# Kernel tuning notes

Measured on AMD Instinct MI355X. Metric: run time of the kernel, lower is better.

The kernel has to match this reference:

```python
import jax, jax.numpy as jnp
import numpy as np

EPS = 1e-6  # flax nn.LayerNorm default epsilon


def excl_cumsum(a, axis):
    c = jnp.roll(jnp.cumsum(a, axis=axis), 1, axis=axis)
    idx = [slice(None)] * a.ndim
    idx[axis] = slice(0, 1)
    return c.at[tuple(idx)].set(0.0)


def mixed_chunk_attn(q, k, v, n_chunks):
    # Mixed chunk linear attention (https://arxiv.org/pdf/2202.10447.pdf)
    if n_chunks == 1:
        mask = jnp.tri(q.shape[1], q.shape[1], -1, dtype=q.dtype)
        qk = jnp.einsum('bls,bms->blm', q, k) * mask
        return jnp.einsum('blm,bme->ble', qk, v)
    B, L = q.shape[:2]
    C = L // n_chunks
    qc = q.reshape(B, n_chunks, C, -1)
    kc = k.reshape(B, n_chunks, C, -1)
    vc = v.reshape(B, n_chunks, C, -1)
    # global linear attention across chunks (exclusive prefix of kv states)
    kv = excl_cumsum(jnp.einsum('bgcs,bgce->bgse', kc, vc), axis=1)
    glob = jnp.einsum('bgcs,bgse->bgce', qc, kv)
    # local strictly-causal quadratic attention within each chunk
    mask = jnp.tri(C, C, -1, dtype=q.dtype)
    qk = jnp.einsum('bgns,bgms->bgnm', qc, kc) * mask
    loc = jnp.einsum('bgnm,bgme->bgne', qk, vc)
    return (glob + loc).reshape(B, L, -1)


def ln_normalize(x):
    mu = jnp.mean(x, axis=-1, keepdims=True)
    var = jnp.mean(jnp.square(x - mu), axis=-1, keepdims=True)
    return (x - mu) * jax.lax.rsqrt(var + EPS)


def fwblock(x, labels, weights, W1, b1, W2, b2, ln_scale, ln_bias, Wu, bu, step_sizes, n_chunks):
    B, L, D = x.shape
    F = W1.shape[1]

    # slow-weight forward with zero perturbations; grad wrt perturbations gives
    # per-token gradients at each layer's output (rank-one fast-weight updates).
    def slow_loss(p1, p3, p_scale, p_bias):
        h1 = x @ W1 + b1 + p1                    # FWDense(4D) + output perturbation
        h2 = jnp.square(jax.nn.relu(h1))         # FWSquaredRelu (paramless)
        h3 = h2 @ W2 + b2 + p3                   # FWDense(D) + output perturbation
        h4 = ln_normalize(h3) * (ln_scale + p_scale) + (ln_bias + p_bias)
        logits = h4 @ Wu + bu
        ll = -jnp.sum(jax.nn.log_softmax(logits) * labels, axis=-1)
        loss = jnp.sum(weights * ll) / jnp.maximum(jnp.sum(weights), 1e-8)
        return loss, h2

    zeros = (jnp.zeros((B, L, F), x.dtype), jnp.zeros((B, L, D), x.dtype),
             jnp.zeros((B, L, D), x.dtype), jnp.zeros((B, L, D), x.dtype))
    (g1, g3, g_scale, g_bias), h2_slow = jax.grad(
        slow_loss, argnums=(0, 1, 2, 3), has_aux=True)(*zeros)

    # fast-weight forward: rank-one weight updates expressed as causal linear attn
    x1 = x @ W1 + b1 - step_sizes[0] * mixed_chunk_attn(x, x, g1, n_chunks)
    x2 = jnp.square(jax.nn.relu(x1))             # step_sizes[1] unused (no params)
    x3 = x2 @ W2 + b2 - step_sizes[2] * mixed_chunk_attn(x2, h2_slow, g3, n_chunks)
    fast_scale = ln_scale - step_sizes[3] * excl_cumsum(g_scale, axis=1)
    fast_bias = ln_bias - step_sizes[3] * excl_cumsum(g_bias, axis=1)
    x4 = ln_normalize(x3) * fast_scale + fast_bias
    return x4 @ Wu + bu


def setup_inputs():
    key = jax.random.key(0)
    ks = jax.random.split(key, 6)
    B, L, D, V = 2, 2048, 1024, 8192
    F = 4 * D
    x = jax.random.normal(ks[0], (B, L, D), jnp.float32)
    labels = jax.random.uniform(ks[1], (B, L, V), jnp.float32)
    weights = jnp.ones((B, L), jnp.float32)
    W1 = jax.random.normal(ks[2], (D, F), jnp.float32) / np.sqrt(D).astype(np.float32)
    b1 = jnp.zeros((F,), jnp.float32)
    W2 = jax.random.normal(ks[3], (F, D), jnp.float32) / np.sqrt(F).astype(np.float32)
    b2 = jnp.zeros((D,), jnp.float32)
    ln_scale = jnp.ones((D,), jnp.float32)
    ln_bias = jnp.zeros((D,), jnp.float32)
    Wu = jax.random.normal(ks[4], (D, V), jnp.float32) / np.sqrt(D).astype(np.float32)
    bu = jnp.zeros((V,), jnp.float32)
    step_sizes = jnp.full((4,), 0.01, jnp.float32)
    return dict(x=x, labels=labels, weights=weights, W1=W1, b1=b1, W2=W2, b2=b2,
                ln_scale=ln_scale, ln_bias=ln_bias, Wu=Wu, bu=bu,
                step_sizes=step_sizes, n_chunks=16)


def reference(x, labels, weights, W1, b1, W2, b2, ln_scale, ln_bias, Wu, bu, step_sizes, n_chunks):
    return fwblock(x, labels, weights, W1, b1, W2, b2, ln_scale, ln_bias, Wu, bu, step_sizes, n_chunks)
```

## Files before the change

kernel.cpp:

```cpp
#include <hip/hip_runtime.h>
#include <cstdint>

typedef unsigned short ushort_t;
typedef __bf16 bf16x8 __attribute__((ext_vector_type(8)));
typedef float f32x4 __attribute__((ext_vector_type(4)));

__device__ __forceinline__ ushort_t f2bf(float f) {
  union { float f; unsigned int u; } v; v.f = f;
  unsigned int u = v.u;
  unsigned int r = (u + 0x7fffu + ((u >> 16) & 1u)) >> 16;
  return (ushort_t)r;
}
__device__ __forceinline__ float bf2f(ushort_t u) {
  union { unsigned int u; float f; } v; v.u = ((unsigned int)u) << 16; return v.f;
}

#define GLOAD16(gp, lp)                                                              \
  __builtin_amdgcn_global_load_lds(                                                  \
      reinterpret_cast<const __attribute__((address_space(1))) unsigned int*>(       \
          reinterpret_cast<uintptr_t>(gp)),                                          \
      reinterpret_cast<__attribute__((address_space(3))) unsigned int*>(             \
          reinterpret_cast<uintptr_t>(lp)),                                          \
      16, 0, 0)

struct GemmP {
  const ushort_t* A; const ushort_t* B;
  int M, N, K;
  long long sA, sB;
  float* outf;   long long sOutF;
  ushort_t* outb; long long sOutB;
  ushort_t* outb2;
  const float* bias;
  const float* auxf; long long sAuxF;
  const ushort_t* auxb;
  const float* steps;
  float* part; int ksplit, Kc, Tt;
};

template <int EPI>
__global__ __launch_bounds__(256) void gemm_bt(GemmP p) {
  const int nwg = gridDim.x * gridDim.y;
  const int orig = blockIdx.y * gridDim.x + blockIdx.x;
  const int xcd = orig & 7, loc = orig >> 3;
  const int q = nwg >> 3, r = nwg & 7;
  const int wg = (xcd < r) ? (xcd * (q + 1) + loc) : (r * (q + 1) + (xcd - r) * q + loc);
  int mt, nt;
  if (EPI == 7) {
    int t_ = wg;
    mt = (int)((sqrtf(8.f * t_ + 1.f) - 1.f) * 0.5f);
    while ((mt + 1) * (mt + 2) / 2 <= t_) mt++;
    while (mt * (mt + 1) / 2 > t_) mt--;
    nt = t_ - mt * (mt + 1) / 2;
  } else {
    nt = wg % gridDim.x; mt = wg / gridDim.x;
  }
  const int m0 = mt * 128, n0 = nt * 128;

  int bz = blockIdx.z, ks = 0;
  if (EPI == 6 || EPI == 7) { bz = blockIdx.z / p.ksplit; ks = blockIdx.z % p.ksplit; }

  const ushort_t* A = p.A + (size_t)bz * p.sA;
  const ushort_t* B = p.B + (size_t)bz * p.sB;

  int kbeg = 0, kend = p.K;
  if (EPI == 6 || EPI == 7) { kbeg = ks * p.Kc; kend = kbeg + p.Kc; }
  else if (EPI == 4 || EPI == 5) kend = min(p.K, m0 + 128);

  __shared__ ushort_t sA[3 * 128 * 32];
  __shared__ ushort_t sB[3 * 128 * 32];

  const int tid = threadIdx.x;
  const int wid = tid >> 6, lane = tid & 63;
  const int wm = wid >> 1, wn = wid & 1;

  f32x4 acc[4][4];
#pragma unroll
  for (int i = 0; i < 4; i++)
#pragma unroll
    for (int j = 0; j < 4; j++) acc[i][j] = f32x4{0.f, 0.f, 0.f, 0.f};

  const int lr = lane >> 2;
  const int lc = (lane & 3) * 8;
  const int rA0 = wid * 16 + lr;
  const int rA1 = 64 + wid * 16 + lr;
  const ushort_t* gA0 = A + (size_t)(m0 + rA0) * p.K + lc;
  const ushort_t* gA1 = A + (size_t)(m0 + rA1) * p.K + lc;
  const ushort_t* gB0 = B + (size_t)(n0 + rA0) * p.K + lc;
  const ushort_t* gB1 = B + (size_t)(n0 + rA1) * p.K + lc;
  ushort_t* lA0 = &sA[wid * 512];
  ushort_t* lA1 = &sA[(4 + wid) * 512];
  ushort_t* lB0 = &sB[wid * 512];
  ushort_t* lB1 = &sB[(4 + wid) * 512];

  const int fr = lane & 15;
  const int kb = (lane >> 4) * 8;

  const int nIter = (kend - kbeg) >> 5;
  auto stage = [&](int t, int buf) {
    const int kk = kbeg + t * 32;
    const int o = buf * 4096;
    GLOAD16(gA0 + kk, lA0 + o);
    GLOAD16(gA1 + kk, lA1 + o);
    GLOAD16(gB0 + kk, lB0 + o);
    GLOAD16(gB1 + kk, lB1 + o);
  };
  stage(0, 0);
  if (nIter > 1) stage(1, 1);

  for (int t = 0; t < nIter; ++t) {
    if (t + 1 < nIter) { asm volatile("s_waitcnt vmcnt(4)" ::: "memory"); }
    else               { asm volatile("s_waitcnt vmcnt(0)" ::: "memory"); }
    __builtin_amdgcn_s_barrier();
    __builtin_amdgcn_sched_barrier(0);
    if (t + 2 < nIter) stage(t + 2, (t + 2) % 3);
    const int co = (t % 3) * 4096;
    bf16x8 av[4], bv[4];
#pragma unroll
    for (int i = 0; i < 4; i++) {
      av[i] = *reinterpret_cast<const bf16x8*>(&sA[co + (wm * 64 + i * 16 + fr) * 32 + kb]);
      bv[i] = *reinterpret_cast<const bf16x8*>(&sB[co + (wn * 64 + i * 16 + fr) * 32 + kb]);
    }
#pragma unroll
    for (int i = 0; i < 4; i++)
#pragma unroll
      for (int j = 0; j < 4; j++)
        acc[i][j] = __builtin_amdgcn_mfma_f32_16x16x32_bf16(av[i], bv[j], acc[i][j], 0, 0, 0);
  }

  const int fq = lane >> 4;
  float ss = 0.f;
  if (EPI == 4) ss = p.steps[0];
  else if (EPI == 5) ss = p.steps[2];
  float* outf = p.outf ? p.outf + (size_t)bz * p.sOutF : nullptr;
  ushort_t* outb = p.outb ? p.outb + (size_t)bz * p.sOutB : nullptr;
  ushort_t* outb2 = p.outb2;
  const float* auxf = p.auxf ? p.auxf + (size_t)bz * p.sAuxF : nullptr;
  const ushort_t* auxb = p.auxb ? p.auxb + (size_t)bz * p.sAuxF : nullptr;
  float* partT = nullptr;
  if (EPI == 6) partT = p.part + (size_t)blockIdx.z * p.M * p.N;
  if (EPI == 7) partT = p.part + ((size_t)blockIdx.z * p.Tt + wg) * 16384;

#pragma unroll
  for (int i = 0; i < 4; i++) {
#pragma unroll
    for (int j = 0; j < 4; j++) {
#pragma unroll
      for (int r2 = 0; r2 < 4; r2++) {
        int lrow = wm * 64 + i * 16 + fq * 4 + r2;
        int lcol = wn * 64 + j * 16 + fr;
        int row = m0 + lrow, col = n0 + lcol;
        size_t g = (size_t)row * p.N + col;
        float v = acc[i][j][r2];
        if (EPI == 0) {
          outf[g] = v + (p.bias ? p.bias[col] : 0.f);
        } else if (EPI == 8) {
          outb[g] = f2bf(v + p.bias[col]);
        } else if (EPI == 1) {
          v += p.bias[col];
          outb[g] = f2bf(v);
          float rl = fmaxf(v, 0.f);
          outb2[g] = f2bf(rl * rl);
        } else if (EPI == 2) {
          outb[g] = f2bf(v * 2.f * sqrtf(bf2f(p.auxb[g])));
        } else if (EPI == 4) {
          float x1 = bf2f(auxb[g]) - ss * v;
          float rl = fmaxf(x1, 0.f);
          outb[g] = f2bf(rl * rl);
        } else if (EPI == 5) {
          outf[g] = auxf[g] - ss * v;
        } else if (EPI == 6) {
          partT[g] = v;
        } else if (EPI == 7) {
          partT[lrow * 128 + lcol] = v;
        }
      }
    }
  }
}

__global__ __launch_bounds__(256) void k_comb(const float* part, const float* bias, float* out,
                                              int N, size_t MN, int S) {
  size_t e = ((size_t)blockIdx.x * 256 + threadIdx.x) * 4;
  if (e >= MN) return;
  float4 s = *(const float4*)(part + e);
  for (int p_ = 1; p_ < S; p_++) {
    float4 v = *(const float4*)(part + (size_t)p_ * MN + e);
    s.x += v.x; s.y += v.y; s.z += v.z; s.w += v.w;
  }
  if (bias) {
    int col = (int)(e % (size_t)N);
    s.x += bias[col]; s.y += bias[col + 1]; s.z += bias[col + 2]; s.w += bias[col + 3];
  }
  *(float4*)(out + e) = s;
}

__global__ __launch_bounds__(256) void k_combtri(const float* part, ushort_t* out, int Tt, int S,
                                                 int L) {
  int t = blockIdx.x, bz = blockIdx.y;
  int mt = (int)((sqrtf(8.f * t + 1.f) - 1.f) * 0.5f);
  while ((mt + 1) * (mt + 2) / 2 <= t) mt++;
  while (mt * (mt + 1) / 2 > t) mt--;
  int nt = t - mt * (mt + 1) / 2;
  const float* pb = part + ((size_t)bz * S * Tt + t) * 16384;
  ushort_t* ob = out + (size_t)bz * L * L;
  for (int e4 = threadIdx.x; e4 < 4096; e4 += 256) {
    int e = e4 * 4;
    float4 s = *(const float4*)(pb + e);
    for (int p_ = 1; p_ < S; p_++) {
      float4 v = *(const float4*)(pb + (size_t)p_ * Tt * 16384 + e);
      s.x += v.x; s.y += v.y; s.z += v.z; s.w += v.w;
    }
    int lr = e >> 7, lc2 = e & 127;
    int row = mt * 128 + lr, col = nt * 128 + lc2;
    ushort4 o;
    o.x = (col < row) ? f2bf(s.x) : (ushort_t)0;
    o.y = (col + 1 < row) ? f2bf(s.y) : (ushort_t)0;
    o.z = (col + 2 < row) ? f2bf(s.z) : (ushort_t)0;
    o.w = (col + 3 < row) ? f2bf(s.w) : (ushort_t)0;
    *(ushort4*)(&ob[(size_t)row * L + col]) = o;
  }
}

__global__ __launch_bounds__(256) void k_conv(const float* in, ushort_t* out, size_t n) {
  size_t i = ((size_t)blockIdx.x * 256 + threadIdx.x) * 4;
  if (i >= n) return;
  float4 v = *(const float4*)(in + i);
  out[i] = f2bf(v.x); out[i + 1] = f2bf(v.y); out[i + 2] = f2bf(v.z); out[i + 3] = f2bf(v.w);
}

__global__ __launch_bounds__(256) void k_tconv(const float* in, ushort_t* out, int R, int C) {
  __shared__ float t[32][33];
  int c0 = blockIdx.x * 32, r0 = blockIdx.y * 32;
  int tx = threadIdx.x & 31, ty = threadIdx.x >> 5;
#pragma unroll
  for (int i = ty; i < 32; i += 8) t[i][tx] = in[(size_t)(r0 + i) * C + c0 + tx];
  __syncthreads();
#pragma unroll
  for (int i = ty; i < 32; i += 8) out[(size_t)(c0 + i) * R + r0 + tx] = f2bf(t[tx][i]);
}

__global__ __launch_bounds__(256) void k_tb2b(const ushort_t* in, ushort_t* out, int L, int C) {
  __shared__ ushort_t t[32][33];
  int b = blockIdx.z;
  const ushort_t* ib = in + (size_t)b * L * C;
  ushort_t* ob = out + (size_t)b * C * L;
  int c0 = blockIdx.x * 32, l0 = blockIdx.y * 32;
  int tx = threadIdx.x & 31, ty = threadIdx.x >> 5;
#pragma unroll
  for (int i = ty; i < 32; i += 8) t[i][tx] = ib[(size_t)(l0 + i) * C + c0 + tx];
  __syncthreads();
#pragma unroll
  for (int i = ty; i < 32; i += 8) ob[(size_t)(c0 + i) * L + l0 + tx] = t[tx][i];
}

__device__ __forceinline__ void blockRed2(float& a, float& b, float* red) {
#pragma unroll
  for (int o = 32; o; o >>= 1) { a += __shfl_down(a, o); b += __shfl_down(b, o); }
  int w = threadIdx.x >> 6;
  if ((threadIdx.x & 63) == 0) { red[w] = a; red[4 + w] = b; }
  __syncthreads();
  a = red[0] + red[1] + red[2] + red[3];
  b = red[4] + red[5] + red[6] + red[7];
  __syncthreads();
}

__global__ __launch_bounds__(256) void k_lnfwd(const float* X, const float* sc, const float* bi,
                                               float* nout, float* rstd, ushort_t* yb, int D) {
  __shared__ float red[8];
  int row = blockIdx.x;
  const float* x = X + (size_t)row * D;
  float s = 0.f, s2 = 0.f;
  for (int d = threadIdx.x; d < D; d += 256) { float v = x[d]; s += v; s2 += v * v; }
  blockRed2(s, s2, red);
  float mu = s / D;
  float var = s2 / D - mu * mu;
  float rs = rsqrtf(var + 1e-6f);
  for (int d = threadIdx.x; d < D; d += 256) {
    float nv = (x[d] - mu) * rs;
    nout[(size_t)row * D + d] = nv;
    yb[(size_t)row * D + d] = f2bf(nv * sc[d] + bi[d]);
  }
  if (threadIdx.x == 0) rstd[row] = rs;
}

__global__ __launch_bounds__(256) void k_lnfwd2(const float* X, const float* fs, const float* fb,
                                                ushort_t* yb, int D) {
  __shared__ float red[8];
  int row = blockIdx.x;
  const float* x = X + (size_t)row * D;
  float s = 0.f, s2 = 0.f;
  for (int d = threadIdx.x; d < D; d += 256) { float v = x[d]; s += v; s2 += v * v; }
  blockRed2(s, s2, red);
  float mu = s / D;
  float var = s2 / D - mu * mu;
  float rs = rsqrtf(var + 1e-6f);
  for (int d = threadIdx.x; d < D; d += 256) {
    size_t g = (size_t)row * D + d;
    float nv = (x[d] - mu) * rs;
    yb[g] = f2bf(nv * fs[g] + fb[g]);
  }
}

__global__ __launch_bounds__(256) void k_lnbwd(const float* G, const float* nn, const float* rstd,
                                               const float* sc, ushort_t* g3b, float* gsc, int D) {
  __shared__ float red[8];
  int row = blockIdx.x;
  const float* g = G + (size_t)row * D;
  const float* n_ = nn + (size_t)row * D;
  float sa = 0.f, sb = 0.f;
  for (int d = threadIdx.x; d < D; d += 256) {
    float dn = g[d] * sc[d];
    sa += dn; sb += dn * n_[d];
  }
  blockRed2(sa, sb, red);
  float a = sa / D, b = sb / D, rs = rstd[row];
  for (int d = threadIdx.x; d < D; d += 256) {
    size_t gi = (size_t)row * D + d;
    float dn = g[d] * sc[d];
    g3b[gi] = f2bf(rs * (dn - a - n_[d] * b));
    gsc[gi] = g[d] * n_[d];
  }
}

__global__ __launch_bounds__(256) void k_wsum(const float* w, float* o, int n) {
  __shared__ float red[4];
  float s = 0.f;
  for (int i = threadIdx.x; i < n; i += 256) s += w[i];
#pragma unroll
  for (int d = 32; d; d >>= 1) s += __shfl_down(s, d);
  if ((threadIdx.x & 63) == 0) red[threadIdx.x >> 6] = s;
  __syncthreads();
  if (threadIdx.x == 0) o[0] = fmaxf(red[0] + red[1] + red[2] + red[3], 1e-8f);
}

__global__ __launch_bounds__(256) void k_softgrad(const ushort_t* logits, const float* labels,
                                                  const float* w, const float* wsum,
                                                  ushort_t* dlb, int V) {
  __shared__ float lrow[8192];
  __shared__ float red[8];
  int row = blockIdx.x;
  const ushort_t* l = logits + (size_t)row * V;
  const float* y = labels + (size_t)row * V;
  float m = -3.4e38f, t = 0.f;
  for (int v = threadIdx.x; v < V; v += 256) {
    float lv = bf2f(l[v]);
    lrow[v] = lv;
    m = fmaxf(m, lv);
    t += y[v];
  }
#pragma unroll
  for (int o = 32; o; o >>= 1) { m = fmaxf(m, __shfl_down(m, o)); t += __shfl_down(t, o); }
  int wv = threadIdx.x >> 6;
  if ((threadIdx.x & 63) == 0) { red[wv] = m; red[4 + wv] = t; }
  __syncthreads();
  m = fmaxf(fmaxf(red[0], red[1]), fmaxf(red[2], red[3]));
  t = red[4] + red[5] + red[6] + red[7];
  __syncthreads();
  float s = 0.f;
  for (int v = threadIdx.x; v < V; v += 256) s += expf(lrow[v] - m);
#pragma unroll
  for (int o = 32; o; o >>= 1) s += __shfl_down(s, o);
  if ((threadIdx.x & 63) == 0) red[wv] = s;
  __syncthreads();
  s = red[0] + red[1] + red[2] + red[3];
  float c = w[row] / wsum[0];
  float invs = 1.f / s;
  for (int v = threadIdx.x; v < V; v += 256) {
    size_t g = (size_t)row * V + v;
    dlb[g] = f2bf(c * (expf(lrow[v] - m) * invs * t - y[v]));
  }
}

__global__ __launch_bounds__(256) void k_scanpart(const float* gs, const float* gb, float* ps,
                                                  float* pb, int L, int D) {
  int d = blockIdx.x * 256 + threadIdx.x;
  int seg = blockIdx.y, b = blockIdx.z;
  const int SEGL = L / 16;
  size_t base = ((size_t)b * L + seg * SEGL) * D + d;
  float s1 = 0.f, s2 = 0.f;
  for (int i = 0; i < SEGL; i++) { s1 += gs[base + (size_t)i * D]; s2 += gb[base + (size_t)i * D]; }
  size_t pi = ((size_t)b * 16 + seg) * D + d;
  ps[pi] = s1; pb[pi] = s2;
}

__global__ __launch_bounds__(256) void k_scanapply(const float* gs, const float* gb,
                                                   const float* ps, const float* pb,
                                                   const float* sc, const float* bi,
                                                   const float* steps, float* fs, float* fb,
                                                   int L, int D) {
  int d = blockIdx.x * 256 + threadIdx.x;
  int seg = blockIdx.y, b = blockIdx.z;
  const int SEGL = L / 16;
  float ss = steps[3];
  float rs_ = 0.f, rb_ = 0.f;
  for (int s = 0; s < seg; s++) {
    size_t pi = ((size_t)b * 16 + s) * D + d;
    rs_ += ps[pi]; rb_ += pb[pi];
  }
  float s0 = sc[d], b0 = bi[d];
  size_t base = ((size_t)b * L + seg * SEGL) * D + d;
  for (int i = 0; i < SEGL; i++) {
    size_t g = base + (size_t)i * D;
    fs[g] = s0 - ss * rs_;
    fb[g] = b0 - ss * rb_;
    rs_ += gs[g]; rb_ += gb[g];
  }
}

extern "C" void kernel_launch(void* const* d_in, const int* in_sizes, int n_in, void* d_out,
                              int out_size, void* d_ws, size_t ws_size, hipStream_t stream) {
  const float* x        = (const float*)d_in[0];
  const float* labels   = (const float*)d_in[1];
  const float* weights  = (const float*)d_in[2];
  const float* W1       = (const float*)d_in[3];
  const float* b1       = (const float*)d_in[4];
  const float* W2       = (const float*)d_in[5];
  const float* b2       = (const float*)d_in[6];
  const float* ln_scale = (const float*)d_in[7];
  const float* ln_bias  = (const float*)d_in[8];
  const float* Wu       = (const float*)d_in[9];
  const float* bu       = (const float*)d_in[10];
  const float* steps    = (const float*)d_in[11];

  const int BL = in_sizes[2];
  const int D  = in_sizes[7];
  const int F  = in_sizes[4];
  const int V  = in_sizes[10];
  const int Bb = 2, L = BL / Bb;
  const int Tt = (L / 128) * (L / 128 + 1) / 2;

  char* ws = (char*)d_ws;
  size_t off = 0;
  auto take = [&](size_t b) { char* p = ws + off; off = (off + b + 255) & ~(size_t)255; return p; };

  ushort_t* xb   = (ushort_t*)take((size_t)BL * D * 2);
  ushort_t* w1t  = (ushort_t*)take((size_t)F * D * 2);
  ushort_t* w2t  = (ushort_t*)take((size_t)D * F * 2);
  ushort_t* w2b  = (ushort_t*)take((size_t)F * D * 2);
  ushort_t* wut  = (ushort_t*)take((size_t)V * D * 2);
  ushort_t* wub  = (ushort_t*)take((size_t)D * V * 2);
  ushort_t* H1b  = (ushort_t*)take((size_t)BL * F * 2);
  ushort_t* H2b  = (ushort_t*)take((size_t)BL * F * 2);
  float*    H3   = (float*)take((size_t)BL * D * 4);
  float*    nbuf = (float*)take((size_t)BL * D * 4);
  float*    rstd = (float*)take((size_t)BL * 4);
  ushort_t* h4b  = (ushort_t*)take((size_t)BL * D * 2);
  float*    wsumb= (float*)take(256);
  float*    G4   = (float*)take((size_t)BL * D * 4);
  float*    gsc  = (float*)take((size_t)BL * D * 4);
  ushort_t* g3b  = (ushort_t*)take((size_t)BL * D * 2);
  ushort_t* g3t  = (ushort_t*)take((size_t)BL * D * 2);
  float*    fs   = (float*)take((size_t)BL * D * 4);
  float*    fb   = (float*)take((size_t)BL * D * 4);
  ushort_t* x4b  = (ushort_t*)take((size_t)BL * D * 2);
  float*    psc  = (float*)take((size_t)Bb * 16 * D * 4);
  float*    pbi  = (float*)take((size_t)Bb * 16 * D * 4);
  char* poolA = take((size_t)BL * V * 4);
  ushort_t* logitsb = (ushort_t*)poolA;
  float*    partA  = (float*)poolA;
  ushort_t* g1b = (ushort_t*)poolA;
  ushort_t* g1t = (ushort_t*)(poolA + (size_t)BL * F * 2);
  ushort_t* S1b = (ushort_t*)(poolA + (size_t)BL * F * 4);
  ushort_t* x2b = (ushort_t*)(poolA + (size_t)BL * F * 4 + (size_t)Bb * L * L * 2);
  char* poolB = take((size_t)BL * V * 2);
  ushort_t* dlb = (ushort_t*)poolB;
  float*    partS1 = (float*)poolB;
  ushort_t* S2b = (ushort_t*)poolB;
  float*    X3  = (float*)(poolB + (size_t)Bb * L * L * 2);
  float*    x3  = (float*)(poolB + (size_t)Bb * L * L * 2 + (size_t)BL * D * 4);

  dim3 blk(256);
  const size_t MN_D = (size_t)BL * D;

  k_conv<<<dim3((unsigned)((size_t)BL * D / 1024)), blk, 0, stream>>>(x, xb, (size_t)BL * D);
  k_tconv<<<dim3(F / 32, D / 32), blk, 0, stream>>>(W1, w1t, D, F);
  k_tconv<<<dim3(D / 32, F / 32), blk, 0, stream>>>(W2, w2t, F, D);
  k_conv<<<dim3((unsigned)((size_t)F * D / 1024)), blk, 0, stream>>>(W2, w2b, (size_t)F * D);
  k_tconv<<<dim3(V / 32, D / 32), blk, 0, stream>>>(Wu, wut, D, V);
  k_conv<<<dim3((unsigned)((size_t)D * V / 1024)), blk, 0, stream>>>(Wu, wub, (size_t)D * V);

  GemmP p;
  auto clr = [&]() { p = GemmP{}; };

  clr(); p.A = xb; p.B = w1t; p.M = BL; p.N = F; p.K = D;
  p.outb = H1b; p.outb2 = H2b; p.bias = b1;
  gemm_bt<1><<<dim3(F / 128, BL / 128, 1), blk, 0, stream>>>(p);
  clr(); p.A = H2b; p.B = w2t; p.M = BL; p.N = D; p.K = F;
  p.part = partA; p.ksplit = 4; p.Kc = F / 4;
  gemm_bt<6><<<dim3(D / 128, BL / 128, 4), blk, 0, stream>>>(p);
  k_comb<<<dim3((unsigned)(MN_D / 1024)), blk, 0, stream>>>(partA, b2, H3, D, MN_D, 4);
  k_lnfwd<<<dim3(BL), blk, 0, stream>>>(H3, ln_scale, ln_bias, nbuf, rstd, h4b, D);
  clr(); p.A = h4b; p.B = wut; p.M = BL; p.N = V; p.K = D; p.outb = logitsb; p.bias = bu;
  gemm_bt<8><<<dim3(V / 128, BL / 128, 1), blk, 0, stream>>>(p);
  k_wsum<<<dim3(1), blk, 0, stream>>>(weights, wsumb, BL);
  k_softgrad<<<dim3(BL), blk, 0, stream>>>(logitsb, labels, weights, wsumb, dlb, V);
  clr(); p.A = dlb; p.B = wub; p.M = BL; p.N = D; p.K = V;
  p.part = partA; p.ksplit = 4; p.Kc = V / 4;
  gemm_bt<6><<<dim3(D / 128, BL / 128, 4), blk, 0, stream>>>(p);
  k_comb<<<dim3((unsigned)(MN_D / 1024)), blk, 0, stream>>>(partA, nullptr, G4, D, MN_D, 4);
  k_lnbwd<<<dim3(BL), blk, 0, stream>>>(G4, nbuf, rstd, ln_scale, g3b, gsc, D);
  clr(); p.A = g3b; p.B = w2b; p.M = BL; p.N = F; p.K = D; p.outb = g1b; p.auxb = H2b;
  gemm_bt<2><<<dim3(F / 128, BL / 128, 1), blk, 0, stream>>>(p);
  k_tb2b<<<dim3(F / 32, L / 32, Bb), blk, 0, stream>>>(g1b, g1t, L, F);
  k_tb2b<<<dim3(D / 32, L / 32, Bb), blk, 0, stream>>>(g3b, g3t, L, D);
  clr(); p.A = xb; p.B = xb; p.M = L; p.N = L; p.K = D;
  p.sA = (long long)L * D; p.sB = (long long)L * D;
  p.part = partS1; p.ksplit = 2; p.Kc = D / 2; p.Tt = Tt;
  gemm_bt<7><<<dim3(Tt, 1, Bb * 2), blk, 0, stream>>>(p);
  k_combtri<<<dim3(Tt, Bb), blk, 0, stream>>>(partS1, S1b, Tt, 2, L);
  clr(); p.A = S1b; p.B = g1t; p.M = L; p.N = F; p.K = L;
  p.sA = (long long)L * L; p.sB = (long long)F * L;
  p.outb = x2b; p.sOutB = (long long)L * F; p.auxb = H1b; p.sAuxF = (long long)L * F;
  p.steps = steps;
  gemm_bt<4><<<dim3(F / 128, L / 128, Bb), blk, 0, stream>>>(p);
  clr(); p.A = x2b; p.B = w2t; p.M = BL; p.N = D; p.K = F;
  p.part = partA; p.ksplit = 4; p.Kc = F / 4;
  gemm_bt<6><<<dim3(D / 128, BL / 128, 4), blk, 0, stream>>>(p);
  k_comb<<<dim3((unsigned)(MN_D / 1024)), blk, 0, stream>>>(partA, b2, X3, D, MN_D, 4);
  clr(); p.A = x2b; p.B = H2b; p.M = L; p.N = L; p.K = F;
  p.sA = (long long)L * F; p.sB = (long long)L * F;
  p.part = partA; p.ksplit = 2; p.Kc = F / 2; p.Tt = Tt;
  gemm_bt<7><<<dim3(Tt, 1, Bb * 2), blk, 0, stream>>>(p);
  k_combtri<<<dim3(Tt, Bb), blk, 0, stream>>>(partA, S2b, Tt, 2, L);
  clr(); p.A = S2b; p.B = g3t; p.M = L; p.N = D; p.K = L;
  p.sA = (long long)L * L; p.sB = (long long)D * L;
  p.outf = x3; p.sOutF = (long long)L * D; p.auxf = X3; p.sAuxF = (long long)L * D; p.steps = steps;
  gemm_bt<5><<<dim3(D / 128, L / 128, Bb), blk, 0, stream>>>(p);
  k_scanpart<<<dim3(D / 256, 16, Bb), blk, 0, stream>>>(gsc, G4, psc, pbi, L, D);
  k_scanapply<<<dim3(D / 256, 16, Bb), blk, 0, stream>>>(gsc, G4, psc, pbi, ln_scale, ln_bias,
                                                         steps, fs, fb, L, D);
  k_lnfwd2<<<dim3(BL), blk, 0, stream>>>(x3, fs, fb, x4b, D);
  clr(); p.A = x4b; p.B = wut; p.M = BL; p.N = V; p.K = D; p.outf = (float*)d_out; p.bias = bu;
  gemm_bt<0><<<dim3(V / 128, BL / 128, 1), blk, 0, stream>>>(p);
}
```

Before: 1.188 ms.

## Add 256x256 tiled 512-thread GEMM with swizzled LDS for most matmuls

Adds a new GEMM kernel that computes 256x256 output tiles with 8 waves per workgroup and an XOR-swizzled LDS layout. Almost all GEMM launches move to it, including the triangular S1/S2 products, whose partial-tile buffers and combine kernel now use 256-wide tiles. The old 128-tile kernel stays only for the x3 update (EPI 5) and is simplified to that case. The S2 triangular product goes from a K-split of 2 to 4. The larger tiles aim to raise data reuse per LDS and global load and to reduce bank conflicts. In exchange the kernel uses more registers and dynamic LDS, launches fewer workgroups, and the K-split of 4 for S2 needs a larger partial buffer.

After: 1.157 ms. 1.03x faster.

```diff
diff --git a/kernel.cpp b/kernel.cpp
--- a/kernel.cpp
+++ b/kernel.cpp
@@ -38,12 +38,12 @@
 };
 
 template <int EPI>
-__global__ __launch_bounds__(256) void gemm_bt(GemmP p) {
+__global__ __launch_bounds__(512, 2) void gemm256(GemmP p) {
   const int nwg = gridDim.x * gridDim.y;
   const int orig = blockIdx.y * gridDim.x + blockIdx.x;
   const int xcd = orig & 7, loc = orig >> 3;
-  const int q = nwg >> 3, r = nwg & 7;
-  const int wg = (xcd < r) ? (xcd * (q + 1) + loc) : (r * (q + 1) + (xcd - r) * q + loc);
+  const int q8 = nwg >> 3, r8 = nwg & 7;
+  const int wg = (xcd < r8) ? (xcd * (q8 + 1) + loc) : (r8 * (q8 + 1) + (xcd - r8) * q8 + loc);
   int mt, nt;
   if (EPI == 7) {
     int t_ = wg;
@@ -54,7 +54,7 @@
   } else {
     nt = wg % gridDim.x; mt = wg / gridDim.x;
   }
-  const int m0 = mt * 128, n0 = nt * 128;
+  const int m0 = mt * 256, n0 = nt * 256;
 
   int bz = blockIdx.z, ks = 0;
   if (EPI == 6 || EPI == 7) { bz = blockIdx.z / p.ksplit; ks = blockIdx.z % p.ksplit; }
@@ -64,41 +64,48 @@
 
   int kbeg = 0, kend = p.K;
   if (EPI == 6 || EPI == 7) { kbeg = ks * p.Kc; kend = kbeg + p.Kc; }
-  else if (EPI == 4 || EPI == 5) kend = min(p.K, m0 + 128);
-
-  __shared__ ushort_t sA[3 * 128 * 32];
-  __shared__ ushort_t sB[3 * 128 * 32];
+  else if (EPI == 4) kend = min(p.K, m0 + 256);
+
+  extern __shared__ ushort_t smem[];
+  ushort_t* sA = smem;
+  ushort_t* sB = smem + 3 * 8192;
 
   const int tid = threadIdx.x;
   const int wid = tid >> 6, lane = tid & 63;
-  const int wm = wid >> 1, wn = wid & 1;
-
-  f32x4 acc[4][4];
-#pragma unroll
-  for (int i = 0; i < 4; i++)
+  const int wm = wid >> 2, wn = wid & 3;
+
+  f32x4 acc[8][4];
+#pragma unroll
+  for (int i = 0; i < 8; i++)
 #pragma unroll
     for (int j = 0; j < 4; j++) acc[i][j] = f32x4{0.f, 0.f, 0.f, 0.f};
 
   const int lr = lane >> 2;
-  const int lc = (lane & 3) * 8;
-  const int rA0 = wid * 16 + lr;
-  const int rA1 = 64 + wid * 16 + lr;
-  const ushort_t* gA0 = A + (size_t)(m0 + rA0) * p.K + lc;
-  const ushort_t* gA1 = A + (size_t)(m0 + rA1) * p.K + lc;
-  const ushort_t* gB0 = B + (size_t)(n0 + rA0) * p.K + lc;
-  const ushort_t* gB1 = B + (size_t)(n0 + rA1) * p.K + lc;
+  const int lcsw = (((lane & 3) ^ ((lr >> 1) & 3)) * 8);
+  const int rT0 = wid * 16 + lr;
+  const int rT1 = 128 + wid * 16 + lr;
+  const ushort_t* gA0 = A + (size_t)(m0 + rT0) * p.K + lcsw;
+  const ushort_t* gA1 = A + (size_t)(m0 + rT1) * p.K + lcsw;
+  const ushort_t* gB0 = B + (size_t)(n0 + rT0) * p.K + lcsw;
+  const ushort_t* gB1 = B + (size_t)(n0 + rT1) * p.K + lcsw;
   ushort_t* lA0 = &sA[wid * 512];
-  ushort_t* lA1 = &sA[(4 + wid) * 512];
+  ushort_t* lA1 = &sA[(8 + wid) * 512];
   ushort_t* lB0 = &sB[wid * 512];
-  ushort_t* lB1 = &sB[(4 + wid) * 512];
+  ushort_t* lB1 = &sB[(8 + wid) * 512];
 
   const int fr = lane & 15;
-  const int kb = (lane >> 4) * 8;
+  const int q = lane >> 4;
+  const int slot = (q ^ ((fr >> 1) & 3)) * 8;
+  int offA[8], offB[4];
+#pragma unroll
+  for (int i = 0; i < 8; i++) offA[i] = (wm * 8 + i) * 512 + fr * 32 + slot;
+#pragma unroll
+  for (int j = 0; j < 4; j++) offB[j] = (wn * 4 + j) * 512 + fr * 32 + slot;
 
   const int nIter = (kend - kbeg) >> 5;
   auto stage = [&](int t, int buf) {
     const int kk = kbeg + t * 32;
-    const int o = buf * 4096;
+    const int o = buf * 8192;
     GLOAD16(gA0 + kk, lA0 + o);
     GLOAD16(gA1 + kk, lA1 + o);
     GLOAD16(gB0 + kk, lB0 + o);
@@ -113,40 +120,37 @@
     __builtin_amdgcn_s_barrier();
     __builtin_amdgcn_sched_barrier(0);
     if (t + 2 < nIter) stage(t + 2, (t + 2) % 3);
-    const int co = (t % 3) * 4096;
-    bf16x8 av[4], bv[4];
-#pragma unroll
-    for (int i = 0; i < 4; i++) {
-      av[i] = *reinterpret_cast<const bf16x8*>(&sA[co + (wm * 64 + i * 16 + fr) * 32 + kb]);
-      bv[i] = *reinterpret_cast<const bf16x8*>(&sB[co + (wn * 64 + i * 16 + fr) * 32 + kb]);
-    }
-#pragma unroll
-    for (int i = 0; i < 4; i++)
+    const int co = (t % 3) * 8192;
+    bf16x8 av[8], bv[4];
+#pragma unroll
+    for (int j = 0; j < 4; j++) bv[j] = *reinterpret_cast<const bf16x8*>(&sB[co + offB[j]]);
+#pragma unroll
+    for (int i = 0; i < 8; i++) {
+      av[i] = *reinterpret_cast<const bf16x8*>(&sA[co + offA[i]]);
 #pragma unroll
       for (int j = 0; j < 4; j++)
         acc[i][j] = __builtin_amdgcn_mfma_f32_16x16x32_bf16(av[i], bv[j], acc[i][j], 0, 0, 0);
-  }
-
-  const int fq = lane >> 4;
+    }
+  }
+
+  const int fq = q;
   float ss = 0.f;
   if (EPI == 4) ss = p.steps[0];
-  else if (EPI == 5) ss = p.steps[2];
   float* outf = p.outf ? p.outf + (size_t)bz * p.sOutF : nullptr;
   ushort_t* outb = p.outb ? p.outb + (size_t)bz * p.sOutB : nullptr;
   ushort_t* outb2 = p.outb2;
-  const float* auxf = p.auxf ? p.auxf + (size_t)bz * p.sAuxF : nullptr;
   const ushort_t* auxb = p.auxb ? p.auxb + (size_t)bz * p.sAuxF : nullptr;
   float* partT = nullptr;
   if (EPI == 6) partT = p.part + (size_t)blockIdx.z * p.M * p.N;
-  if (EPI == 7) partT = p.part + ((size_t)blockIdx.z * p.Tt + wg) * 16384;
-
-#pragma unroll
-  for (int i = 0; i < 4; i++) {
+  if (EPI == 7) partT = p.part + ((size_t)blockIdx.z * p.Tt + wg) * 65536;
+
+#pragma unroll
+  for (int i = 0; i < 8; i++) {
 #pragma unroll
     for (int j = 0; j < 4; j++) {
 #pragma unroll
       for (int r2 = 0; r2 < 4; r2++) {
-        int lrow = wm * 64 + i * 16 + fq * 4 + r2;
+        int lrow = wm * 128 + i * 16 + fq * 4 + r2;
         int lcol = wn * 64 + j * 16 + fr;
         int row = m0 + lrow, col = n0 + lcol;
         size_t g = (size_t)row * p.N + col;
@@ -161,17 +165,118 @@
           float rl = fmaxf(v, 0.f);
           outb2[g] = f2bf(rl * rl);
         } else if (EPI == 2) {
-          outb[g] = f2bf(v * 2.f * sqrtf(bf2f(p.auxb[g])));
+          outb[g] = f2bf(v * 2.f * sqrtf(bf2f(auxb[g])));
         } else if (EPI == 4) {
           float x1 = bf2f(auxb[g]) - ss * v;
           float rl = fmaxf(x1, 0.f);
           outb[g] = f2bf(rl * rl);
-        } else if (EPI == 5) {
-          outf[g] = auxf[g] - ss * v;
         } else if (EPI == 6) {
           partT[g] = v;
         } else if (EPI == 7) {
-          partT[lrow * 128 + lcol] = v;
+          partT[lrow * 256 + lcol] = v;
+        }
+      }
+    }
+  }
+}
+
+template <int EPI>
+__global__ __launch_bounds__(256) void gemm_bt(GemmP p) {
+  const int nwg = gridDim.x * gridDim.y;
+  const int orig = blockIdx.y * gridDim.x + blockIdx.x;
+  const int xcd = orig & 7, loc = orig >> 3;
+  const int q = nwg >> 3, r = nwg & 7;
+  const int wg = (xcd < r) ? (xcd * (q + 1) + loc) : (r * (q + 1) + (xcd - r) * q + loc);
+  const int nt = wg % gridDim.x, mt = wg / gridDim.x;
+  const int m0 = mt * 128, n0 = nt * 128;
+  const int bz = blockIdx.z;
+
+  const ushort_t* A = p.A + (size_t)bz * p.sA;
+  const ushort_t* B = p.B + (size_t)bz * p.sB;
+
+  int kend = p.K;
+  if (EPI == 5) kend = min(p.K, m0 + 128);
+
+  __shared__ ushort_t sA[3 * 128 * 32];
+  __shared__ ushort_t sB[3 * 128 * 32];
+
+  const int tid = threadIdx.x;
+  const int wid = tid >> 6, lane = tid & 63;
+  const int wm = wid >> 1, wn = wid & 1;
+
+  f32x4 acc[4][4];
+#pragma unroll
+  for (int i = 0; i < 4; i++)
+#pragma unroll
+    for (int j = 0; j < 4; j++) acc[i][j] = f32x4{0.f, 0.f, 0.f, 0.f};
+
+  const int lr = lane >> 2;
+  const int lc = (lane & 3) * 8;
+  const int rA0 = wid * 16 + lr;
+  const int rA1 = 64 + wid * 16 + lr;
+  const ushort_t* gA0 = A + (size_t)(m0 + rA0) * p.K + lc;
+  const ushort_t* gA1 = A + (size_t)(m0 + rA1) * p.K + lc;
+  const ushort_t* gB0 = B + (size_t)(n0 + rA0) * p.K + lc;
+  const ushort_t* gB1 = B + (size_t)(n0 + rA1) * p.K + lc;
+  ushort_t* lA0 = &sA[wid * 512];
+  ushort_t* lA1 = &sA[(4 + wid) * 512];
+  ushort_t* lB0 = &sB[wid * 512];
+  ushort_t* lB1 = &sB[(4 + wid) * 512];
+
+  const int fr = lane & 15;
+  const int kb = (lane >> 4) * 8;
+
+  const int nIter = kend >> 5;
+  auto stage = [&](int t, int buf) {
+    const int kk = t * 32;
+    const int o = buf * 4096;
+    GLOAD16(gA0 + kk, lA0 + o);
+    GLOAD16(gA1 + kk, lA1 + o);
+    GLOAD16(gB0 + kk, lB0 + o);
+    GLOAD16(gB1 + kk, lB1 + o);
+  };
+  stage(0, 0);
+  if (nIter > 1) stage(1, 1);
+
+  for (int t = 0; t < nIter; ++t) {
+    if (t + 1 < nIter) { asm volatile("s_waitcnt vmcnt(4)" ::: "memory"); }
+    else               { asm volatile("s_waitcnt vmcnt(0)" ::: "memory"); }
+    __builtin_amdgcn_s_barrier();
+    __builtin_amdgcn_sched_barrier(0);
+    if (t + 2 < nIter) stage(t + 2, (t + 2) % 3);
+    const int co = (t % 3) * 4096;
+    bf16x8 av[4], bv[4];
+#pragma unroll
+    for (int i = 0; i < 4; i++) {
+      av[i] = *reinterpret_cast<const bf16x8*>(&sA[co + (wm * 64 + i * 16 + fr) * 32 + kb]);
+      bv[i] = *reinterpret_cast<const bf16x8*>(&sB[co + (wn * 64 + i * 16 + fr) * 32 + kb]);
+    }
+#pragma unroll
+    for (int i = 0; i < 4; i++)
+#pragma unroll
+      for (int j = 0; j < 4; j++)
+        acc[i][j] = __builtin_amdgcn_mfma_f32_16x16x32_bf16(av[i], bv[j], acc[i][j], 0, 0, 0);
+  }
+
+  const int fq = lane >> 4;
+  float ss = (EPI == 5) ? p.steps[2] : 0.f;
+  float* outf = p.outf ? p.outf + (size_t)bz * p.sOutF : nullptr;
+  const float* auxf = p.auxf ? p.auxf + (size_t)bz * p.sAuxF : nullptr;
+
+#pragma unroll
+  for (int i = 0; i < 4; i++) {
+#pragma unroll
+    for (int j = 0; j < 4; j++) {
+#pragma unroll
+      for (int r2 = 0; r2 < 4; r2++) {
+        int row = m0 + wm * 64 + i * 16 + fq * 4 + r2;
+        int col = n0 + wn * 64 + j * 16 + fr;
+        size_t g = (size_t)row * p.N + col;
+        float v = acc[i][j][r2];
+        if (EPI == 5) {
+          outf[g] = auxf[g] - ss * v;
+        } else {
+          outf[g] = v + (p.bias ? p.bias[col] : 0.f);
         }
       }
     }
@@ -201,17 +306,17 @@
   while ((mt + 1) * (mt + 2) / 2 <= t) mt++;
   while (mt * (mt + 1) / 2 > t) mt--;
   int nt = t - mt * (mt + 1) / 2;
-  const float* pb = part + ((size_t)bz * S * Tt + t) * 16384;
+  const float* pb = part + ((size_t)bz * S * Tt + t) * 65536;
   ushort_t* ob = out + (size_t)bz * L * L;
-  for (int e4 = threadIdx.x; e4 < 4096; e4 += 256) {
+  for (int e4 = threadIdx.x; e4 < 16384; e4 += 256) {
     int e = e4 * 4;
     float4 s = *(const float4*)(pb + e);
     for (int p_ = 1; p_ < S; p_++) {
-      float4 v = *(const float4*)(pb + (size_t)p_ * Tt * 16384 + e);
+      float4 v = *(const float4*)(pb + (size_t)p_ * Tt * 65536 + e);
       s.x += v.x; s.y += v.y; s.z += v.z; s.w += v.w;
     }
-    int lr = e >> 7, lc2 = e & 127;
-    int row = mt * 128 + lr, col = nt * 128 + lc2;
+    int lr = e >> 8, lc2 = e & 255;
+    int row = mt * 256 + lr, col = nt * 256 + lc2;
     ushort4 o;
     o.x = (col < row) ? f2bf(s.x) : (ushort_t)0;
     o.y = (col + 1 < row) ? f2bf(s.y) : (ushort_t)0;
@@ -427,7 +532,8 @@
   const int F  = in_sizes[4];
   const int V  = in_sizes[10];
   const int Bb = 2, L = BL / Bb;
-  const int Tt = (L / 128) * (L / 128 + 1) / 2;
+  const int T2t = (L / 256) * (L / 256 + 1) / 2;
+  const unsigned SMEM = 3 * 8192 * 2 * 2;
 
   char* ws = (char*)d_ws;
   size_t off = 0;
@@ -469,7 +575,7 @@
   float*    X3  = (float*)(poolB + (size_t)Bb * L * L * 2);
   float*    x3  = (float*)(poolB + (size_t)Bb * L * L * 2 + (size_t)BL * D * 4);
 
-  dim3 blk(256);
+  dim3 blk(256), blk5(512);
   const size_t MN_D = (size_t)BL * D;
 
   k_conv<<<dim3((unsigned)((size_t)BL * D / 1024)), blk, 0, stream>>>(x, xb, (size_t)BL * D);
@@ -484,44 +590,44 @@
 
   clr(); p.A = xb; p.B = w1t; p.M = BL; p.N = F; p.K = D;
   p.outb = H1b; p.outb2 = H2b; p.bias = b1;
-  gemm_bt<1><<<dim3(F / 128, BL / 128, 1), blk, 0, stream>>>(p);
+  gemm256<1><<<dim3(F / 256, BL / 256, 1), blk5, SMEM, stream>>>(p);
   clr(); p.A = H2b; p.B = w2t; p.M = BL; p.N = D; p.K = F;
   p.part = partA; p.ksplit = 4; p.Kc = F / 4;
-  gemm_bt<6><<<dim3(D / 128, BL / 128, 4), blk, 0, stream>>>(p);
+  gemm256<6><<<dim3(D / 256, BL / 256, 4), blk5, SMEM, stream>>>(p);
   k_comb<<<dim3((unsigned)(MN_D / 1024)), blk, 0, stream>>>(partA, b2, H3, D, MN_D, 4);
   k_lnfwd<<<dim3(BL), blk, 0, stream>>>(H3, ln_scale, ln_bias, nbuf, rstd, h4b, D);
   clr(); p.A = h4b; p.B = wut; p.M = BL; p.N = V; p.K = D; p.outb = logitsb; p.bias = bu;
-  gemm_bt<8><<<dim3(V / 128, BL / 128, 1), blk, 0, stream>>>(p);
+  gemm256<8><<<dim3(V / 256, BL / 256, 1), blk5, SMEM, stream>>>(p);
   k_wsum<<<dim3(1), blk, 0, stream>>>(weights, wsumb, BL);
   k_softgrad<<<dim3(BL), blk, 0, stream>>>(logitsb, labels, weights, wsumb, dlb, V);
   clr(); p.A = dlb; p.B = wub; p.M = BL; p.N = D; p.K = V;
   p.part = partA; p.ksplit = 4; p.Kc = V / 4;
-  gemm_bt<6><<<dim3(D / 128, BL / 128, 4), blk, 0, stream>>>(p);
+  gemm256<6><<<dim3(D / 256, BL / 256, 4), blk5, SMEM, stream>>>(p);
   k_comb<<<dim3((unsigned)(MN_D / 1024)), blk, 0, stream>>>(partA, nullptr, G4, D, MN_D, 4);
   k_lnbwd<<<dim3(BL), blk, 0, stream>>>(G4, nbuf, rstd, ln_scale, g3b, gsc, D);
   clr(); p.A = g3b; p.B = w2b; p.M = BL; p.N = F; p.K = D; p.outb = g1b; p.auxb = H2b;
-  gemm_bt<2><<<dim3(F / 128, BL / 128, 1), blk, 0, stream>>>(p);
+  gemm256<2><<<dim3(F / 256, BL / 256, 1), blk5, SMEM, stream>>>(p);
   k_tb2b<<<dim3(F / 32, L / 32, Bb), blk, 0, stream>>>(g1b, g1t, L, F);
   k_tb2b<<<dim3(D / 32, L / 32, Bb), blk, 0, stream>>>(g3b, g3t, L, D);
   clr(); p.A = xb; p.B = xb; p.M = L; p.N = L; p.K = D;
   p.sA = (long long)L * D; p.sB = (long long)L * D;
-  p.part = partS1; p.ksplit = 2; p.Kc = D / 2; p.Tt = Tt;
-  gemm_bt<7><<<dim3(Tt, 1, Bb * 2), blk, 0, stream>>>(p);
-  k_combtri<<<dim3(Tt, Bb), blk, 0, stream>>>(partS1, S1b, Tt, 2, L);
+  p.part = partS1; p.ksplit = 2; p.Kc = D / 2; p.Tt = T2t;
+  gemm256<7><<<dim3(T2t, 1, Bb * 2), blk5, SMEM, stream>>>(p);
+  k_combtri<<<dim3(T2t, Bb), blk, 0, stream>>>(partS1, S1b, T2t, 2, L);
   clr(); p.A = S1b; p.B = g1t; p.M = L; p.N = F; p.K = L;
   p.sA = (long long)L * L; p.sB = (long long)F * L;
   p.outb = x2b; p.sOutB = (long long)L * F; p.auxb = H1b; p.sAuxF = (long long)L * F;
   p.steps = steps;
-  gemm_bt<4><<<dim3(F / 128, L / 128, Bb), blk, 0, stream>>>(p);
+  gemm256<4><<<dim3(F / 256, L / 256, Bb), blk5, SMEM, stream>>>(p);
   clr(); p.A = x2b; p.B = w2t; p.M = BL; p.N = D; p.K = F;
   p.part = partA; p.ksplit = 4; p.Kc = F / 4;
-  gemm_bt<6><<<dim3(D / 128, BL / 128, 4), blk, 0, stream>>>(p);
+  gemm256<6><<<dim3(D / 256, BL / 256, 4), blk5, SMEM, stream>>>(p);
   k_comb<<<dim3((unsigned)(MN_D / 1024)), blk, 0, stream>>>(partA, b2, X3, D, MN_D, 4);
   clr(); p.A = x2b; p.B = H2b; p.M = L; p.N = L; p.K = F;
   p.sA = (long long)L * F; p.sB = (long long)L * F;
-  p.part = partA; p.ksplit = 2; p.Kc = F / 2; p.Tt = Tt;
-  gemm_bt<7><<<dim3(Tt, 1, Bb * 2), blk, 0, stream>>>(p);
-  k_combtri<<<dim3(Tt, Bb), blk, 0, stream>>>(partA, S2b, Tt, 2, L);
+  p.part = partA; p.ksplit = 4; p.Kc = F / 4; p.Tt = T2t;
+  gemm256<7><<<dim3(T2t, 1, Bb * 4), blk5, SMEM, stream>>>(p);
+  k_combtri<<<dim3(T2t, Bb), blk, 0, stream>>>(partA, S2b, T2t, 4, L);
   clr(); p.A = S2b; p.B = g3t; p.M = L; p.N = D; p.K = L;
   p.sA = (long long)L * L; p.sB = (long long)D * L;
   p.outf = x3; p.sOutF = (long long)L * D; p.auxf = X3; p.sAuxF = (long long)L * D; p.steps = steps;
@@ -531,5 +637,5 @@
                                                          steps, fs, fb, L, D);
   k_lnfwd2<<<dim3(BL), blk, 0, stream>>>(x3, fs, fb, x4b, D);
   clr(); p.A = x4b; p.B = wut; p.M = BL; p.N = V; p.K = D; p.outf = (float*)d_out; p.bias = bu;
-  gemm_bt<0><<<dim3(V / 128, BL / 128, 1), blk, 0, stream>>>(p);
-}
+  gemm256<0><<<dim3(V / 256, BL / 256, 1), blk5, SMEM, stream>>>(p);
+}
```
